# Performance work log

Measured on AMD Instinct MI355X. Metric: run time of the kernel, lower is better.

The kernel has to match this reference:

```python
import jax, jax.numpy as jnp
import numpy as np

B, N, I, H = 1024, 16, 256, 1024
V = 0.08  # init_var


def setup_inputs() -> dict:
    key = jax.random.key(0)
    ks = jax.random.split(key, 16)
    inp = jax.random.normal(ks[0], (B, N, I), jnp.float32)
    p = (jax.random.uniform(ks[1], (B, N, N)) > 0.3).astype(jnp.float32)
    phis = jnp.maximum(p, jnp.eye(N, dtype=jnp.float32)[None])  # ensure >=1 valid slot per row
    u = lambda k, s: jax.random.uniform(k, s, jnp.float32, -V, V)
    return {
        'input': inp, 'phis': phis,
        'init_token': jnp.zeros((I,), jnp.float32),
        'W1': u(ks[2], (H, H)), 'W2': u(ks[3], (H, H)), 'v': u(ks[4], (H, 1)),
        'Wih_e': u(ks[5], (3 * H, I)), 'Whh_e': u(ks[6], (3 * H, H)),
        'bih_e': u(ks[7], (3 * H,)), 'bhh_e': u(ks[8], (3 * H,)),
        'Wih_d': u(ks[9], (3 * H, I)), 'Whh_d': u(ks[10], (3 * H, H)),
        'bih_d': u(ks[11], (3 * H,)), 'bhh_d': u(ks[12], (3 * H,)),
    }


def gru_cell(x, h, Wih, Whh, bih, bhh):
    # torch.nn.GRUCell semantics; gate order [r, z, n]
    gi = x @ Wih.T + bih
    gh = h @ Whh.T + bhh
    ir, iz, ig = jnp.split(gi, 3, -1)
    hr, hz, hg = jnp.split(gh, 3, -1)
    r = jax.nn.sigmoid(ir + hr)
    z = jax.nn.sigmoid(iz + hz)
    g = jnp.tanh(ig + r * hg)
    return (1 - z) * g + z * h


def masked_softmax(mask, u):
    # faithful to softmax_m: mask before max, mask exps, normalize
    um = u * mask
    m = jnp.max(um, 1, keepdims=True)
    e = jnp.exp(um - m) * mask
    return e / jnp.sum(e, 1, keepdims=True)


def reference(input, phis, init_token, W1, W2, v,
              Wih_e, Whh_e, bih_e, bhh_e, Wih_d, Whh_d, bih_d, bhh_d):
    # gating scalar t_n = phis[:, n, n-1]; t_0 := 1 (no-op at step 0)
    t_gate = jnp.concatenate(
        [jnp.ones((B, 1), input.dtype), jnp.diagonal(phis, -1, 1, 2)], axis=1).T  # (N, B)

    # ---- Encoder ----
    def enc_step(h, xs):
        x, t = xs
        h = gru_cell(x, t[:, None] * h, Wih_e, Whh_e, bih_e, bhh_e)
        return h, h

    _, henc = jax.lax.scan(enc_step, jnp.zeros((B, H), input.dtype),
                           (input.transpose(1, 0, 2), t_gate))
    hidden_encoder = henc.transpose(1, 0, 2)  # (B, N, H)

    # ---- Decoder ----
    Ns = phis.sum(2)                                             # (B, N)
    idx_seq = ((Ns + jnp.arange(N)[None] - 1) % N).astype(jnp.int32)  # (B, N)
    bidx = jnp.arange(B)
    hidden0 = hidden_encoder[bidx, ((Ns[:, 0] - 1) % N).astype(jnp.int32)]  # (B, H)
    W1xe = jnp.einsum('bnh,hk->bnk', hidden_encoder, W1)         # (B, N, H)
    start = jnp.broadcast_to(init_token, (B, I))

    def dec_step(carry, xs):
        hidden, inp_step = carry
        t, idx, mask = xs
        init_h = hidden_encoder[bidx, idx]
        hidden = t[:, None] * hidden + (1 - t)[:, None] * init_h
        inp_step = t[:, None] * inp_step + (1 - t)[:, None] * start
        hidden = gru_cell(inp_step, hidden, Wih_d, Whh_d, bih_d, bhh_d)
        u = jnp.squeeze(jnp.tanh(W1xe + (hidden @ W2)[:, None, :]) @ v, -1)  # (B, N)
        attn = masked_softmax(mask, u)
        inp_step = jnp.einsum('bn,bni->bi', attn, input)
        return (hidden, inp_step), attn

    _, attns = jax.lax.scan(dec_step, (hidden0, start),
                            (t_gate, idx_seq.T, phis.transpose(1, 0, 2)))
    return attns.transpose(1, 0, 2)  # (B, N, N)
```

## Files before the change

kernel.cpp:

```cpp
#include <hip/hip_runtime.h>
#include <math.h>

#define B_  1024
#define N_  16
#define I_  256
#define H_  1024
#define H3_ 3072

typedef _Float16 f16;
typedef _Float16 f16x4 __attribute__((ext_vector_type(4)));
typedef _Float16 f16x8 __attribute__((ext_vector_type(8)));
typedef float    f32x4 __attribute__((ext_vector_type(4)));

__device__ __forceinline__ float sigmoidf_(float x) { return 1.f / (1.f + expf(-x)); }

__device__ __forceinline__ void lds_write_row(f16* dst, int row, int s, f16x8 vv)
{
    int key = (row >> 1) & 3;
    int g0  = (((s & 1) * 2 + 0) ^ key);
    int g1  = (((s & 1) * 2 + 1) ^ key);
    f16x4 lo = {vv[0], vv[1], vv[2], vv[3]};
    f16x4 hi = {vv[4], vv[5], vv[6], vv[7]};
    *(f16x4*)((char*)dst + row * 64 + g0 * 16 + (s >> 1) * 8) = lo;
    *(f16x4*)((char*)dst + row * 64 + g1 * 16 + (s >> 1) * 8) = hi;
}

__global__ void precompute_kernel(const float* __restrict__ phis,
                                  float* __restrict__ tg,
                                  int* __restrict__ idx)
{
    int b = blockIdx.x * blockDim.x + threadIdx.x;
    if (b >= B_) return;
    tg[b] = 1.0f;
    for (int t = 1; t < N_; ++t)
        tg[t * B_ + b] = phis[(size_t)b * N_ * N_ + t * N_ + (t - 1)];
    tg[16 * B_ + b] = 0.0f;
    for (int t = 0; t < N_; ++t) {
        float ns = 0.f;
        for (int k = 0; k < N_; ++k) ns += phis[(size_t)b * N_ * N_ + t * N_ + k];
        int nsi = (int)(ns + 0.5f);
        idx[b * N_ + t] = (nsi + t - 1) % N_;
    }
}

__global__ void cast_kernel(const float* __restrict__ in, f16* __restrict__ out, int n)
{
    int i = blockIdx.x * blockDim.x + threadIdx.x;
    if (i < n) out[i] = (f16)in[i];
}

__global__ void cast4_kernel(const float* __restrict__ s0, f16* __restrict__ d0, int n0,
                             const float* __restrict__ s1, f16* __restrict__ d1, int n1,
                             const float* __restrict__ s2, f16* __restrict__ d2, int n2,
                             const float* __restrict__ s3, f16* __restrict__ d3, int n3)
{
    int i = blockIdx.x * blockDim.x + threadIdx.x;
    int T0 = n0, T1 = T0 + n1, T2 = T1 + n2, T3 = T2 + n3;
    if (i < T0) d0[i] = (f16)s0[i];
    else if (i < T1) d1[i - T0] = (f16)s1[i - T0];
    else if (i < T2) d2[i - T1] = (f16)s2[i - T1];
    else if (i < T3) d3[i - T2] = (f16)s3[i - T2];
}

__global__ __launch_bounds__(256) void transpose_cast2_kernel(
    const float* __restrict__ in0, f16* __restrict__ out0,
    const float* __restrict__ in1, f16* __restrict__ out1)
{
    const float* in  = blockIdx.z ? in1 : in0;
    f16*        outp = blockIdx.z ? out1 : out0;
    __shared__ float tile[32][33];
    int bx = blockIdx.x * 32, by = blockIdx.y * 32;
    int tx = threadIdx.x & 31, ty = threadIdx.x >> 5;
#pragma unroll
    for (int r = 0; r < 32; r += 8)
        tile[ty + r][tx] = in[(size_t)(by + ty + r) * H_ + bx + tx];
    __syncthreads();
#pragma unroll
    for (int r = 0; r < 32; r += 8)
        outp[(size_t)(bx + ty + r) * H_ + by + tx] = (f16)tile[tx][ty + r];
}

template <typename OutT>
__global__ __launch_bounds__(256) void hgemm_kernel(
    const f16* __restrict__ A, int lda,
    const f16* __restrict__ Bt, int ldb,
    OutT* __restrict__ C, int ldc, int K)
{
    __shared__ char smem[32768];

    const int tid  = threadIdx.x;
    const int lane = tid & 63;
    const int wid  = tid >> 6;
    const int wr   = wid >> 1;
    const int wc   = wid & 1;
    const int rsel = lane & 15;
    const int kb   = lane >> 4;

    int flat = blockIdx.y * gridDim.x + blockIdx.x;
    int nwg  = gridDim.x * gridDim.y;
    int cpx  = nwg >> 3;
    int nf   = (flat & 7) * cpx + (flat >> 3);
    const int n0 = (int)(nf % gridDim.x) * 128;
    const int m0 = (int)(nf / gridDim.x) * 128;

    const int strow0 = tid >> 2;
    const int strow1 = 64 + (tid >> 2);
    const int sts    = tid & 3;

    f32x4 acc[4][4];
#pragma unroll
    for (int m = 0; m < 4; ++m)
#pragma unroll
        for (int n = 0; n < 4; ++n) acc[m][n] = (f32x4)0.f;

    f16x8 sA0, sA1, sB0, sB1;
    f16x8 tA0, tA1, tB0, tB1;
    auto GL0 = [&](int k0) {
        sA0 = *(const f16x8*)(A + (size_t)(m0 + strow0) * lda + k0 + sts * 8);
        sA1 = *(const f16x8*)(A + (size_t)(m0 + strow1) * lda + k0 + sts * 8);
        sB0 = *(const f16x8*)(Bt + (size_t)(n0 + strow0) * ldb + k0 + sts * 8);
        sB1 = *(const f16x8*)(Bt + (size_t)(n0 + strow1) * ldb + k0 + sts * 8);
    };
    auto GL1 = [&](int k0) {
        tA0 = *(const f16x8*)(A + (size_t)(m0 + strow0) * lda + k0 + sts * 8);
        tA1 = *(const f16x8*)(A + (size_t)(m0 + strow1) * lda + k0 + sts * 8);
        tB0 = *(const f16x8*)(Bt + (size_t)(n0 + strow0) * ldb + k0 + sts * 8);
        tB1 = *(const f16x8*)(Bt + (size_t)(n0 + strow1) * ldb + k0 + sts * 8);
    };
    auto LW0 = [&](int c) {
        f16* As_ = (f16*)(smem + c * 8192);
        f16* Bs_ = (f16*)(smem + 16384 + c * 8192);
        lds_write_row(As_, strow0, sts, sA0);
        lds_write_row(As_, strow1, sts, sA1);
        lds_write_row(Bs_, strow0, sts, sB0);
        lds_write_row(Bs_, strow1, sts, sB1);
    };
    auto LW1 = [&](int c) {
        f16* As_ = (f16*)(smem + c * 8192);
        f16* Bs_ = (f16*)(smem + 16384 + c * 8192);
        lds_write_row(As_, strow0, sts, tA0);
        lds_write_row(As_, strow1, sts, tA1);
        lds_write_row(Bs_, strow0, sts, tB0);
        lds_write_row(Bs_, strow1, sts, tB1);
    };
    auto COMP = [&](int c) {
        char* As_ = smem + c * 8192;
        char* Bs_ = smem + 16384 + c * 8192;
        f16x8 af[4], bf[4];
#pragma unroll
        for (int m = 0; m < 4; ++m) {
            int row = wr * 64 + m * 16 + rsel;
            af[m] = *(const f16x8*)(As_ + row * 64 + ((kb ^ ((row >> 1) & 3)) << 4));
        }
#pragma unroll
        for (int n = 0; n < 4; ++n) {
            int row = wc * 64 + n * 16 + rsel;
            bf[n] = *(const f16x8*)(Bs_ + row * 64 + ((kb ^ ((row >> 1) & 3)) << 4));
        }
#pragma unroll
        for (int m = 0; m < 4; ++m)
#pragma unroll
            for (int n = 0; n < 4; ++n)
                acc[m][n] = __builtin_amdgcn_mfma_f32_16x16x32_f16(af[m], bf[n], acc[m][n], 0, 0, 0);
    };

    const int nk = K / 32;
    GL0(0);
    GL1(32);
    LW0(0);
    __syncthreads();

    for (int ks = 0; ks < nk; ks += 2) {
        if (ks + 2 < nk) GL0((ks + 2) * 32);
        COMP(0);
        LW1(1);
        __syncthreads();
        if (ks + 3 < nk) GL1((ks + 3) * 32);
        COMP(1);
        if (ks + 2 < nk) LW0(0);
        __syncthreads();
    }

#pragma unroll
    for (int m = 0; m < 4; ++m) {
        int row0 = m0 + wr * 64 + m * 16 + kb * 4;
#pragma unroll
        for (int n = 0; n < 4; ++n) {
            int col = n0 + wc * 64 + n * 16 + rsel;
#pragma unroll
            for (int r = 0; r < 4; ++r)
                C[(size_t)(row0 + r) * ldc + col] = (OutT)acc[m][n][r];
        }
    }
}

template <int MODE>
__global__ __launch_bounds__(512) void gru_fused_kernel(
    const f16* __restrict__ A1, int lda1,
    const f16* __restrict__ Bt1,
    const f16* __restrict__ A2,
    const f16* __restrict__ Bt2,
    const float* __restrict__ bih, const float* __restrict__ bhh,
    float* __restrict__ h,
    const float* __restrict__ tg_cur,
    const float* __restrict__ tg_next,
    f16* __restrict__ out_a,
    f16* __restrict__ hs)
{
    __shared__ char smem[57344];

    const int tid  = threadIdx.x;
    const int wg   = tid >> 8;
    const int ltid = tid & 255;
    const int lane = tid & 63;
    const int wid4 = (ltid >> 6);
    const int wr   = wid4 >> 1;
    const int wc   = wid4 & 1;
    const int rsel = lane & 15;
    const int kb   = lane >> 4;

    char* base = smem + wg * 28672;

    int flat = blockIdx.y * gridDim.x + blockIdx.x;
    int nf   = (flat & 7) * 64 + (flat >> 3);
    const int j0 = (nf >> 5) * 64;
    const int b0 = (nf & 31) * 32;

    const int strow = ltid >> 2;
    const int sts   = ltid & 3;

    f32x4 acc1[3][2], acc2[3][2];
#pragma unroll
    for (int g = 0; g < 3; ++g)
#pragma unroll
        for (int nt = 0; nt < 2; ++nt) { acc1[g][nt] = (f32x4)0.f; acc2[g][nt] = (f32x4)0.f; }

    f16x8 sA, sB0, sB1, sB2;
    f16x8 tA, tB0, tB1, tB2;
    const f16* Ap;  const f16* Btp;  int ldap, ldbp;
    auto GL0 = [&](int k0) {
        if (ltid < 128) sA = *(const f16x8*)(Ap + (size_t)(b0 + strow) * ldap + k0 + sts * 8);
        sB0 = *(const f16x8*)(Btp + (size_t)(0 * H_ + j0 + strow) * ldbp + k0 + sts * 8);
        sB1 = *(const f16x8*)(Btp + (size_t)(1 * H_ + j0 + strow) * ldbp + k0 + sts * 8);
        sB2 = *(const f16x8*)(Btp + (size_t)(2 * H_ + j0 + strow) * ldbp + k0 + sts * 8);
    };
    auto GL1 = [&](int k0) {
        if (ltid < 128) tA = *(const f16x8*)(Ap + (size_t)(b0 + strow) * ldap + k0 + sts * 8);
        tB0 = *(const f16x8*)(Btp + (size_t)(0 * H_ + j0 + strow) * ldbp + k0 + sts * 8);
        tB1 = *(const f16x8*)(Btp + (size_t)(1 * H_ + j0 + strow) * ldbp + k0 + sts * 8);
        tB2 = *(const f16x8*)(Btp + (size_t)(2 * H_ + j0 + strow) * ldbp + k0 + sts * 8);
    };
    auto LW0 = [&](int c) {
        if (ltid < 128) lds_write_row((f16*)(base + c * 2048), strow, sts, sA);
        f16* Bs_ = (f16*)(base + 4096 + c * 12288);
        lds_write_row(Bs_ + 0 * 64 * 32, strow, sts, sB0);
        lds_write_row(Bs_ + 1 * 64 * 32, strow, sts, sB1);
        lds_write_row(Bs_ + 2 * 64 * 32, strow, sts, sB2);
    };
    auto LW1 = [&](int c) {
        if (ltid < 128) lds_write_row((f16*)(base + c * 2048), strow, sts, tA);
        f16* Bs_ = (f16*)(base + 4096 + c * 12288);
        lds_write_row(Bs_ + 0 * 64 * 32, strow, sts, tB0);
        lds_write_row(Bs_ + 1 * 64 * 32, strow, sts, tB1);
        lds_write_row(Bs_ + 2 * 64 * 32, strow, sts, tB2);
    };
    auto COMP = [&](int c, int phase) {
        char* As_ = base + c * 2048;
        char* Bs_ = base + 4096 + c * 12288;
        int arow = wr * 16 + rsel;
        f16x8 af = *(const f16x8*)(As_ + arow * 64 + ((kb ^ ((arow >> 1) & 3)) << 4));
#pragma unroll
        for (int gg = 0; gg < 3; ++gg)
#pragma unroll
            for (int nt = 0; nt < 2; ++nt) {
                int brow = wc * 32 + nt * 16 + rsel;
                f16x8 bf = *(const f16x8*)(Bs_ + (gg * 64 + brow) * 64 +
                                           ((kb ^ ((brow >> 1) & 3)) << 4));
                if (phase == 0)
                    acc1[gg][nt] = __builtin_amdgcn_mfma_f32_16x16x32_f16(af, bf, acc1[gg][nt], 0, 0, 0);
                else
                    acc2[gg][nt] = __builtin_amdgcn_mfma_f32_16x16x32_f16(af, bf, acc2[gg][nt], 0, 0, 0);
            }
    };

#pragma unroll
    for (int phase = 0; phase < 2; ++phase) {
        Ap   = phase ? A2 : A1;
        Btp  = phase ? Bt2 : Bt1;
        ldap = phase ? H_ : lda1;
        ldbp = phase ? H_ : I_;
        const int Kp   = phase ? H_ : I_;
        const int half = Kp >> 1;
        const int kbeg = wg * half;
        const int nk   = half >> 5;

        GL0(kbeg);
        GL1(kbeg + 32);
        LW0(0);
        __syncthreads();

#pragma unroll
        for (int ks = 0; ks < nk; ks += 2) {
            if (ks + 2 < nk) GL0(kbeg + (ks + 2) * 32);
            COMP(0, phase);
            LW1(1);
            __syncthreads();
            if (ks + 3 < nk) GL1(kbeg + (ks + 3) * 32);
            COMP(1, phase);
            if (ks + 2 < nk) LW0(0);
            __syncthreads();
        }
    }

    f32x4* red = (f32x4*)smem;
    if (wg) {
#pragma unroll
        for (int g = 0; g < 3; ++g)
#pragma unroll
            for (int nt = 0; nt < 2; ++nt) red[ltid * 6 + g * 2 + nt] = acc1[g][nt];
    }
    __syncthreads();
    if (!wg) {
#pragma unroll
        for (int g = 0; g < 3; ++g)
#pragma unroll
            for (int nt = 0; nt < 2; ++nt) acc1[g][nt] += red[ltid * 6 + g * 2 + nt];
    }
    __syncthreads();
    if (wg) {
#pragma unroll
        for (int g = 0; g < 3; ++g)
#pragma unroll
            for (int nt = 0; nt < 2; ++nt) red[ltid * 6 + g * 2 + nt] = acc2[g][nt];
    }
    __syncthreads();

    if (!wg) {
#pragma unroll
        for (int g = 0; g < 3; ++g)
#pragma unroll
            for (int nt = 0; nt < 2; ++nt) acc2[g][nt] += red[ltid * 6 + g * 2 + nt];

#pragma unroll
        for (int nt = 0; nt < 2; ++nt) {
            int j = j0 + wc * 32 + nt * 16 + rsel;
            float br_i = bih[j],          br_h = bhh[j];
            float bz_i = bih[H_ + j],     bz_h = bhh[H_ + j];
            float bg_i = bih[2 * H_ + j], bg_h = bhh[2 * H_ + j];
#pragma unroll
            for (int q = 0; q < 4; ++q) {
                int row = b0 + wr * 16 + kb * 4 + q;
                float r = sigmoidf_(acc1[0][nt][q] + br_i + acc2[0][nt][q] + br_h);
                float z = sigmoidf_(acc1[1][nt][q] + bz_i + acc2[1][nt][q] + bz_h);
                float g = tanhf(acc1[2][nt][q] + bg_i + r * (acc2[2][nt][q] + bg_h));
                float leak;
                if (MODE == 0) leak = tg_cur[row] * h[(size_t)row * H_ + j];
                else           leak = h[(size_t)row * H_ + j];
                float hn = (1.f - z) * g + z * leak;
                h[(size_t)row * H_ + j] = hn;
                if (MODE == 0) {
                    out_a[(size_t)row * (N_ * H_) + j] = (f16)hn;
                    hs[(size_t)row * H_ + j] = (f16)(tg_next[row] * hn);
                } else {
                    out_a[(size_t)row * H_ + j] = (f16)hn;
                }
            }
        }
    }
}

__global__ __launch_bounds__(512) void hgemm64_kernel(
    const f16* __restrict__ A, const f16* __restrict__ Bt, float* __restrict__ C)
{
    __shared__ char smem[32768];

    const int tid  = threadIdx.x;
    const int wg   = tid >> 8;
    const int ltid = tid & 255;
    const int lane = tid & 63;
    const int wid4 = (ltid >> 6);
    const int wr   = wid4 >> 1;
    const int wc   = wid4 & 1;
    const int rsel = lane & 15;
    const int kb   = lane >> 4;

    char* base = smem + wg * 16384;

    int flat = blockIdx.y * gridDim.x + blockIdx.x;
    int nf   = (flat & 7) * 32 + (flat >> 3);
    const int m0 = (nf >> 4) * 64;
    const int n0 = (nf & 15) * 64;

    const int strow = ltid >> 2;
    const int sts   = ltid & 3;

    f32x4 acc[2][2];
#pragma unroll
    for (int m = 0; m < 2; ++m)
#pragma unroll
        for (int n = 0; n < 2; ++n) acc[m][n] = (f32x4)0.f;

    f16x8 sA, sB, tA, tB;
    auto GL0 = [&](int k0) {
        sA = *(const f16x8*)(A + (size_t)(m0 + strow) * H_ + k0 + sts * 8);
        sB = *(const f16x8*)(Bt + (size_t)(n0 + strow) * H_ + k0 + sts * 8);
    };
    auto GL1 = [&](int k0) {
        tA = *(const f16x8*)(A + (size_t)(m0 + strow) * H_ + k0 + sts * 8);
        tB = *(const f16x8*)(Bt + (size_t)(n0 + strow) * H_ + k0 + sts * 8);
    };
    auto LW0 = [&](int c) {
        lds_write_row((f16*)(base + c * 4096), strow, sts, sA);
        lds_write_row((f16*)(base + 8192 + c * 4096), strow, sts, sB);
    };
    auto LW1 = [&](int c) {
        lds_write_row((f16*)(base + c * 4096), strow, sts, tA);
        lds_write_row((f16*)(base + 8192 + c * 4096), strow, sts, tB);
    };
    auto COMP = [&](int c) {
        char* As_ = base + c * 4096;
        char* Bs_ = base + 8192 + c * 4096;
        f16x8 af[2], bf[2];
#pragma unroll
        for (int m = 0; m < 2; ++m) {
            int row = wr * 32 + m * 16 + rsel;
            af[m] = *(const f16x8*)(As_ + row * 64 + ((kb ^ ((row >> 1) & 3)) << 4));
        }
#pragma unroll
        for (int nt = 0; nt < 2; ++nt) {
            int row = wc * 32 + nt * 16 + rsel;
            bf[nt] = *(const f16x8*)(Bs_ + row * 64 + ((kb ^ ((row >> 1) & 3)) << 4));
        }
#pragma unroll
        for (int m = 0; m < 2; ++m)
#pragma unroll
            for (int nt = 0; nt < 2; ++nt)
                acc[m][nt] = __builtin_amdgcn_mfma_f32_16x16x32_f16(af[m], bf[nt], acc[m][nt], 0, 0, 0);
    };

    const int kbeg = wg * 512;
    GL0(kbeg);
    GL1(kbeg + 32);
    LW0(0);
    __syncthreads();

#pragma unroll
    for (int ks = 0; ks < 16; ks += 2) {
        if (ks + 2 < 16) GL0(kbeg + (ks + 2) * 32);
        COMP(0);
        LW1(1);
        __syncthreads();
        if (ks + 3 < 16) GL1(kbeg + (ks + 3) * 32);
        COMP(1);
        if (ks + 2 < 16) LW0(0);
        __syncthreads();
    }

    f32x4* red = (f32x4*)smem;
    if (wg) {
#pragma unroll
        for (int m = 0; m < 2; ++m)
#pragma unroll
            for (int nt = 0; nt < 2; ++nt) red[ltid * 4 + m * 2 + nt] = acc[m][nt];
    }
    __syncthreads();
    if (!wg) {
#pragma unroll
        for (int m = 0; m < 2; ++m)
#pragma unroll
            for (int nt = 0; nt < 2; ++nt) {
                acc[m][nt] += red[ltid * 4 + m * 2 + nt];
                int col = n0 + wc * 32 + nt * 16 + rsel;
#pragma unroll
                for (int q = 0; q < 4; ++q) {
                    int row = m0 + wr * 32 + m * 16 + kb * 4 + q;
                    C[(size_t)row * H_ + col] = acc[m][nt][q];
                }
            }
    }
}

__global__ void dec_init_kernel(float* __restrict__ h, f16* __restrict__ hs,
                                const f16* __restrict__ he, const int* __restrict__ idx,
                                f16* __restrict__ inp, const float* __restrict__ tok)
{
    int i = blockIdx.x * blockDim.x + threadIdx.x;
    int b = i >> 10;
    int j = i & (H_ - 1);
    float v0 = (float)he[(size_t)b * N_ * H_ + (size_t)idx[b * N_] * H_ + j];
    h[i]  = v0;
    hs[i] = (f16)v0;
    if (i < B_ * I_) inp[i] = (f16)tok[i & (I_ - 1)];
}

template <int MIX>
__global__ __launch_bounds__(1024) void attn_kernel(
    const f16*   __restrict__ w1xe,
    const float* __restrict__ hw2,
    const float* __restrict__ v,
    const float* __restrict__ phis,
    const f16*   __restrict__ in16,
    float* __restrict__ out,
    f16*   __restrict__ inp_step,
    int t,
    const float* __restrict__ tg_next,
    const int*   __restrict__ idx_next,
    const f16*   __restrict__ he,
    float* __restrict__ h,
    f16*   __restrict__ hs,
    const float* __restrict__ tok)
{
    int b   = blockIdx.x;
    int tid = threadIdx.x;
    int w   = tid >> 6;
    int l   = tid & 63;
    __shared__ float un[N_];
    __shared__ float attns[N_];

    {
        const f16*   wrow = w1xe + ((size_t)(b * N_ + w)) * H_;
        const float* hwp  = hw2 + (size_t)b * H_;
        f16x8 w0 = *(const f16x8*)(wrow + l * 8);
        f16x8 w1 = *(const f16x8*)(wrow + 512 + l * 8);
        f32x4 h0 = *(const f32x4*)(hwp + l * 8);
        f32x4 h1 = *(const f32x4*)(hwp + l * 8 + 4);
        f32x4 h2 = *(const f32x4*)(hwp + 512 + l * 8);
        f32x4 h3 = *(const f32x4*)(hwp + 512 + l * 8 + 4);
        f32x4 v0 = *(const f32x4*)(v + l * 8);
        f32x4 v1 = *(const f32x4*)(v + l * 8 + 4);
        f32x4 v2 = *(const f32x4*)(v + 512 + l * 8);
        f32x4 v3 = *(const f32x4*)(v + 512 + l * 8 + 4);
        float s = 0.f;
#pragma unroll
        for (int e = 0; e < 4; ++e) {
            s += tanhf((float)w0[e]     + h0[e]) * v0[e];
            s += tanhf((float)w0[e + 4] + h1[e]) * v1[e];
            s += tanhf((float)w1[e]     + h2[e]) * v2[e];
            s += tanhf((float)w1[e + 4] + h3[e]) * v3[e];
        }
#pragma unroll
        for (int off = 32; off; off >>= 1) s += __shfl_down(s, off, 64);
        if (l == 0) un[w] = s;
    }
    __syncthreads();

    if (tid < N_) {
        float mk = phis[(size_t)b * N_ * N_ + t * N_ + tid];
        float um = un[tid] * mk;
        float m = um;
#pragma unroll
        for (int off = 1; off < 16; off <<= 1) m = fmaxf(m, __shfl_xor(m, off, 16));
        float e = expf(um - m) * mk;
        float ssum = e;
#pragma unroll
        for (int off = 1; off < 16; off <<= 1) ssum += __shfl_xor(ssum, off, 16);
        float a = e / ssum;
        attns[tid] = a;
        out[(size_t)b * N_ * N_ + t * N_ + tid] = a;
    }
    __syncthreads();

    if (tid < I_) {
        float acc = 0.f;
#pragma unroll
        for (int n = 0; n < N_; ++n)
            acc += attns[n] * (float)in16[((size_t)b * N_ + n) * I_ + tid];
        if (MIX) {
            float tn = tg_next[b];
            inp_step[(size_t)b * I_ + tid] = (f16)(tn * acc + (1.f - tn) * tok[tid]);
        } else {
            inp_step[(size_t)b * I_ + tid] = (f16)acc;
        }
    }

    if (MIX) {
        float tn = tg_next[b];
        int id = idx_next[b * N_];
        float ih = (float)he[(size_t)b * N_ * H_ + (size_t)id * H_ + tid];
        float hm = tn * h[(size_t)b * H_ + tid] + (1.f - tn) * ih;
        h[(size_t)b * H_ + tid]  = hm;
        hs[(size_t)b * H_ + tid] = (f16)hm;
    }
}

extern "C" void kernel_launch(void* const* d_in, const int* in_sizes, int n_in,
                              void* d_out, int out_size, void* d_ws, size_t ws_size,
                              hipStream_t stream)
{
    const float* input      = (const float*)d_in[0];
    const float* phis       = (const float*)d_in[1];
    const float* init_token = (const float*)d_in[2];
    const float* W1         = (const float*)d_in[3];
    const float* W2         = (const float*)d_in[4];
    const float* v          = (const float*)d_in[5];
    const float* Wih_e      = (const float*)d_in[6];
    const float* Whh_e      = (const float*)d_in[7];
    const float* bih_e      = (const float*)d_in[8];
    const float* bhh_e      = (const float*)d_in[9];
    const float* Wih_d      = (const float*)d_in[10];
    const float* Whh_d      = (const float*)d_in[11];
    const float* bih_d      = (const float*)d_in[12];
    const float* bhh_d      = (const float*)d_in[13];
    float* out = (float*)d_out;

    char* p = (char*)d_ws;
    f16*  he16    = (f16*)p;  p += (size_t)B_ * N_ * H_ * 2;
    f16*  w1xe16  = (f16*)p;  p += (size_t)B_ * N_ * H_ * 2;
    float* h      = (float*)p; p += (size_t)B_ * H_ * 4;
    f16*  hs16    = (f16*)p;  p += (size_t)2 * B_ * H_ * 2;
    f16*  hc16    = (f16*)p;  p += (size_t)B_ * H_ * 2;
    f16*  inp16   = (f16*)p;  p += (size_t)B_ * I_ * 2;
    float* hw2    = (float*)p; p += (size_t)B_ * H_ * 4;
    f16*  in16    = (f16*)p;  p += (size_t)B_ * N_ * I_ * 2;
    f16*  Wih_e16 = (f16*)p;  p += (size_t)H3_ * I_ * 2;
    f16*  Whh_e16 = (f16*)p;  p += (size_t)H3_ * H_ * 2;
    f16*  Wih_d16 = (f16*)p;  p += (size_t)H3_ * I_ * 2;
    f16*  Whh_d16 = (f16*)p;  p += (size_t)H3_ * H_ * 2;
    f16*  W1t16   = (f16*)p;  p += (size_t)H_ * H_ * 2;
    f16*  W2t16   = (f16*)p;  p += (size_t)H_ * H_ * 2;
    float* tg     = (float*)p; p += (size_t)17 * B_ * 4;
    int*   idx    = (int*)p;   p += (size_t)B_ * N_ * 4;

    const size_t BH = (size_t)B_ * H_;
    const int BHBLK = (B_ * H_) / 256;
    const dim3 gru_grid(16, 32);

    precompute_kernel<<<4, 256, 0, stream>>>(phis, tg, idx);

    cast_kernel<<<(B_ * N_ * I_) / 256, 256, 0, stream>>>(input, in16, B_ * N_ * I_);
    cast4_kernel<<<(2 * (H3_ * I_ + H3_ * H_)) / 256, 256, 0, stream>>>(
        Wih_e, Wih_e16, H3_ * I_, Whh_e, Whh_e16, H3_ * H_,
        Wih_d, Wih_d16, H3_ * I_, Whh_d, Whh_d16, H3_ * H_);
    transpose_cast2_kernel<<<dim3(32, 32, 2), 256, 0, stream>>>(W1, W1t16, W2, W2t16);

    hipMemsetAsync(h, 0, BH * 4, stream);
    hipMemsetAsync(hs16, 0, BH * 2, stream);
    for (int t = 0; t < N_; ++t) {
        gru_fused_kernel<0><<<gru_grid, 512, 0, stream>>>(
            in16 + (size_t)t * I_, N_ * I_, Wih_e16,
            hs16 + (size_t)(t & 1) * BH, Whh_e16, bih_e, bhh_e, h,
            tg + (size_t)t * B_, tg + (size_t)(t + 1) * B_,
            he16 + (size_t)t * H_, hs16 + (size_t)((t + 1) & 1) * BH);
    }

    hgemm_kernel<f16><<<dim3(H_ / 128, (B_ * N_) / 128), 256, 0, stream>>>(
        he16, H_, W1t16, H_, w1xe16, H_, H_);

    dec_init_kernel<<<BHBLK, 256, 0, stream>>>(h, hs16, he16, idx, inp16, init_token);
    for (int t = 0; t < N_; ++t) {
        gru_fused_kernel<1><<<gru_grid, 512, 0, stream>>>(
            inp16, I_, Wih_d16,
            hs16, Whh_d16, bih_d, bhh_d, h,
            nullptr, nullptr, hc16, nullptr);
        hgemm64_kernel<<<dim3(16, 16), 512, 0, stream>>>(hc16, W2t16, hw2);
        if (t < N_ - 1)
            attn_kernel<1><<<B_, 1024, 0, stream>>>(
                w1xe16, hw2, v, phis, in16, out, inp16, t,
                tg + (size_t)(t + 1) * B_, idx + (t + 1), he16, h, hs16, init_token);
        else
            attn_kernel<0><<<B_, 1024, 0, stream>>>(
                w1xe16, hw2, v, phis, in16, out, inp16, t,
                tg, idx, he16, h, hs16, init_token);
    }
}
```

Measured before the change: 1.274 ms.

## Split-K the W2 GEMM across grid z and merge GRU r/z accumulators

The per-step hidden@W2 GEMM now uses a grid z-dimension of 2. Each block handles half of K and writes its partial result to its own buffer, and the attention kernel adds the two partials when it loads them. This doubles the block count of a small 256-block GEMM for better occupancy, at the cost of extra workspace and extra global reads in attention. Separately, the GRU kernel accumulates the input and hidden contributions for the r and z gates into shared accumulators, which cuts register use and the size of the cross-wavegroup LDS reduction (one barrier round fewer).

```diff
diff --git a/kernel.cpp b/kernel.cpp
--- a/kernel.cpp
+++ b/kernel.cpp
@@ -229,11 +229,12 @@
     const int strow = ltid >> 2;
     const int sts   = ltid & 3;
 
-    f32x4 acc1[3][2], acc2[3][2];
-#pragma unroll
-    for (int g = 0; g < 3; ++g)
-#pragma unroll
-        for (int nt = 0; nt < 2; ++nt) { acc1[g][nt] = (f32x4)0.f; acc2[g][nt] = (f32x4)0.f; }
+    f32x4 acc_rz[2][2];
+    f32x4 acc_g[2][2];
+#pragma unroll
+    for (int g = 0; g < 2; ++g)
+#pragma unroll
+        for (int nt = 0; nt < 2; ++nt) { acc_rz[g][nt] = (f32x4)0.f; acc_g[g][nt] = (f32x4)0.f; }
 
     f16x8 sA, sB0, sB1, sB2;
     f16x8 tA, tB0, tB1, tB2;
@@ -276,10 +277,12 @@
                 int brow = wc * 32 + nt * 16 + rsel;
                 f16x8 bf = *(const f16x8*)(Bs_ + (gg * 64 + brow) * 64 +
                                            ((kb ^ ((brow >> 1) & 3)) << 4));
-                if (phase == 0)
-                    acc1[gg][nt] = __builtin_amdgcn_mfma_f32_16x16x32_f16(af, bf, acc1[gg][nt], 0, 0, 0);
+                if (gg < 2)
+                    acc_rz[gg][nt] = __builtin_amdgcn_mfma_f32_16x16x32_f16(af, bf, acc_rz[gg][nt], 0, 0, 0);
+                else if (phase == 0)
+                    acc_g[0][nt] = __builtin_amdgcn_mfma_f32_16x16x32_f16(af, bf, acc_g[0][nt], 0, 0, 0);
                 else
-                    acc2[gg][nt] = __builtin_amdgcn_mfma_f32_16x16x32_f16(af, bf, acc2[gg][nt], 0, 0, 0);
+                    acc_g[1][nt] = __builtin_amdgcn_mfma_f32_16x16x32_f16(af, bf, acc_g[1][nt], 0, 0, 0);
             }
     };
 
@@ -315,44 +318,36 @@
     f32x4* red = (f32x4*)smem;
     if (wg) {
 #pragma unroll
-        for (int g = 0; g < 3; ++g)
-#pragma unroll
-            for (int nt = 0; nt < 2; ++nt) red[ltid * 6 + g * 2 + nt] = acc1[g][nt];
+        for (int g = 0; g < 2; ++g)
+#pragma unroll
+            for (int nt = 0; nt < 2; ++nt) {
+                red[ltid * 8 + g * 2 + nt]     = acc_rz[g][nt];
+                red[ltid * 8 + 4 + g * 2 + nt] = acc_g[g][nt];
+            }
     }
     __syncthreads();
+
     if (!wg) {
 #pragma unroll
-        for (int g = 0; g < 3; ++g)
-#pragma unroll
-            for (int nt = 0; nt < 2; ++nt) acc1[g][nt] += red[ltid * 6 + g * 2 + nt];
-    }
-    __syncthreads();
-    if (wg) {
-#pragma unroll
-        for (int g = 0; g < 3; ++g)
-#pragma unroll
-            for (int nt = 0; nt < 2; ++nt) red[ltid * 6 + g * 2 + nt] = acc2[g][nt];
-    }
-    __syncthreads();
-
-    if (!wg) {
-#pragma unroll
-        for (int g = 0; g < 3; ++g)
-#pragma unroll
-            for (int nt = 0; nt < 2; ++nt) acc2[g][nt] += red[ltid * 6 + g * 2 + nt];
+        for (int g = 0; g < 2; ++g)
+#pragma unroll
+            for (int nt = 0; nt < 2; ++nt) {
+                acc_rz[g][nt] += red[ltid * 8 + g * 2 + nt];
+                acc_g[g][nt]  += red[ltid * 8 + 4 + g * 2 + nt];
+            }
 
 #pragma unroll
         for (int nt = 0; nt < 2; ++nt) {
             int j = j0 + wc * 32 + nt * 16 + rsel;
-            float br_i = bih[j],          br_h = bhh[j];
-            float bz_i = bih[H_ + j],     bz_h = bhh[H_ + j];
+            float br = bih[j] + bhh[j];
+            float bz = bih[H_ + j] + bhh[H_ + j];
             float bg_i = bih[2 * H_ + j], bg_h = bhh[2 * H_ + j];
 #pragma unroll
             for (int q = 0; q < 4; ++q) {
                 int row = b0 + wr * 16 + kb * 4 + q;
-                float r = sigmoidf_(acc1[0][nt][q] + br_i + acc2[0][nt][q] + br_h);
-                float z = sigmoidf_(acc1[1][nt][q] + bz_i + acc2[1][nt][q] + bz_h);
-                float g = tanhf(acc1[2][nt][q] + bg_i + r * (acc2[2][nt][q] + bg_h));
+                float r = sigmoidf_(acc_rz[0][nt][q] + br);
+                float z = sigmoidf_(acc_rz[1][nt][q] + bz);
+                float g = tanhf(acc_g[0][nt][q] + bg_i + r * (acc_g[1][nt][q] + bg_h));
                 float leak;
                 if (MODE == 0) leak = tg_cur[row] * h[(size_t)row * H_ + j];
                 else           leak = h[(size_t)row * H_ + j];
@@ -370,7 +365,7 @@
 }
 
 __global__ __launch_bounds__(512) void hgemm64_kernel(
-    const f16* __restrict__ A, const f16* __restrict__ Bt, float* __restrict__ C)
+    const f16* __restrict__ A, const f16* __restrict__ Bt, float* __restrict__ Cp)
 {
     __shared__ char smem[32768];
 
@@ -390,6 +385,7 @@
     int nf   = (flat & 7) * 32 + (flat >> 3);
     const int m0 = (nf >> 4) * 64;
     const int n0 = (nf & 15) * 64;
+    const int kz = blockIdx.z;
 
     const int strow = ltid >> 2;
     const int sts   = ltid & 3;
@@ -438,21 +434,21 @@
                 acc[m][nt] = __builtin_amdgcn_mfma_f32_16x16x32_f16(af[m], bf[nt], acc[m][nt], 0, 0, 0);
     };
 
-    const int kbeg = wg * 512;
+    const int kbeg = kz * 512 + wg * 256;
     GL0(kbeg);
     GL1(kbeg + 32);
     LW0(0);
     __syncthreads();
 
 #pragma unroll
-    for (int ks = 0; ks < 16; ks += 2) {
-        if (ks + 2 < 16) GL0(kbeg + (ks + 2) * 32);
+    for (int ks = 0; ks < 8; ks += 2) {
+        if (ks + 2 < 8) GL0(kbeg + (ks + 2) * 32);
         COMP(0);
         LW1(1);
         __syncthreads();
-        if (ks + 3 < 16) GL1(kbeg + (ks + 3) * 32);
+        if (ks + 3 < 8) GL1(kbeg + (ks + 3) * 32);
         COMP(1);
-        if (ks + 2 < 16) LW0(0);
+        if (ks + 2 < 8) LW0(0);
         __syncthreads();
     }
 
@@ -465,6 +461,7 @@
     }
     __syncthreads();
     if (!wg) {
+        float* C = Cp + (size_t)kz * B_ * H_;
 #pragma unroll
         for (int m = 0; m < 2; ++m)
 #pragma unroll
@@ -496,7 +493,7 @@
 template <int MIX>
 __global__ __launch_bounds__(1024) void attn_kernel(
     const f16*   __restrict__ w1xe,
-    const float* __restrict__ hw2,
+    const float* __restrict__ hw2p,
     const float* __restrict__ v,
     const float* __restrict__ phis,
     const f16*   __restrict__ in16,
@@ -519,13 +516,14 @@
 
     {
         const f16*   wrow = w1xe + ((size_t)(b * N_ + w)) * H_;
-        const float* hwp  = hw2 + (size_t)b * H_;
+        const float* hp0  = hw2p + (size_t)b * H_;
+        const float* hp1  = hw2p + (size_t)B_ * H_ + (size_t)b * H_;
         f16x8 w0 = *(const f16x8*)(wrow + l * 8);
         f16x8 w1 = *(const f16x8*)(wrow + 512 + l * 8);
-        f32x4 h0 = *(const f32x4*)(hwp + l * 8);
-        f32x4 h1 = *(const f32x4*)(hwp + l * 8 + 4);
-        f32x4 h2 = *(const f32x4*)(hwp + 512 + l * 8);
-        f32x4 h3 = *(const f32x4*)(hwp + 512 + l * 8 + 4);
+        f32x4 h0 = *(const f32x4*)(hp0 + l * 8)       + *(const f32x4*)(hp1 + l * 8);
+        f32x4 h1 = *(const f32x4*)(hp0 + l * 8 + 4)   + *(const f32x4*)(hp1 + l * 8 + 4);
+        f32x4 h2 = *(const f32x4*)(hp0 + 512 + l * 8) + *(const f32x4*)(hp1 + 512 + l * 8);
+        f32x4 h3 = *(const f32x4*)(hp0 + 512 + l * 8 + 4) + *(const f32x4*)(hp1 + 512 + l * 8 + 4);
         f32x4 v0 = *(const f32x4*)(v + l * 8);
         f32x4 v1 = *(const f32x4*)(v + l * 8 + 4);
         f32x4 v2 = *(const f32x4*)(v + 512 + l * 8);
@@ -610,7 +608,7 @@
     f16*  hs16    = (f16*)p;  p += (size_t)2 * B_ * H_ * 2;
     f16*  hc16    = (f16*)p;  p += (size_t)B_ * H_ * 2;
     f16*  inp16   = (f16*)p;  p += (size_t)B_ * I_ * 2;
-    float* hw2    = (float*)p; p += (size_t)B_ * H_ * 4;
+    float* hw2p   = (float*)p; p += (size_t)2 * B_ * H_ * 4;
     f16*  in16    = (f16*)p;  p += (size_t)B_ * N_ * I_ * 2;
     f16*  Wih_e16 = (f16*)p;  p += (size_t)H3_ * I_ * 2;
     f16*  Whh_e16 = (f16*)p;  p += (size_t)H3_ * H_ * 2;
@@ -652,14 +650,14 @@
             inp16, I_, Wih_d16,
             hs16, Whh_d16, bih_d, bhh_d, h,
             nullptr, nullptr, hc16, nullptr);
-        hgemm64_kernel<<<dim3(16, 16), 512, 0, stream>>>(hc16, W2t16, hw2);
+        hgemm64_kernel<<<dim3(16, 16, 2), 512, 0, stream>>>(hc16, W2t16, hw2p);
         if (t < N_ - 1)
             attn_kernel<1><<<B_, 1024, 0, stream>>>(
-                w1xe16, hw2, v, phis, in16, out, inp16, t,
+                w1xe16, hw2p, v, phis, in16, out, inp16, t,
                 tg + (size_t)(t + 1) * B_, idx + (t + 1), he16, h, hs16, init_token);
         else
             attn_kernel<0><<<B_, 1024, 0, stream>>>(
-                w1xe16, hw2, v, phis, in16, out, inp16, t,
+                w1xe16, hw2p, v, phis, in16, out, inp16, t,
                 tg, idx, he16, h, hs16, init_token);
     }
 }
```

After: 1.338 ms. 1.05x slower.
